# Kernel tuning notes

Measured on AMD Instinct MI355X. Metric: run time of the kernel, lower is better.

The kernel has to match this reference:

```python
import jax, jax.numpy as jnp
import numpy as np

N_TBINS = 1024
K = 8
B = 32768
IRF_SIGMA = 10.0
PEAK_FACTOR = 5.0
# IRF1DLayer: circular pad (pad_l=N//2, pad_r=N//2-1 for even N) then conv1d with
# flip(irf)  ==  circular convolution with irf followed by roll of -(N-1-N//2).
ROLL_C = N_TBINS - 1 - N_TBINS // 2  # 511


def _wrapped_gaussian(n, mu, sigma):
    # circ_shifted gaussian pulse: wrap tails around the domain, normalize to unit area
    t = np.arange(n, dtype=np.float64)
    g = np.zeros(n, dtype=np.float64)
    for s in (-n, 0, n):
        g += np.exp(-((t - mu + s) ** 2) / (2.0 * sigma ** 2))
    g /= g.sum()
    return jnp.asarray(g, dtype=jnp.float32)


def _circ_conv(x, irf):
    # faithful IRF1DLayer: circular convolution, recentered
    y = jnp.fft.irfft(jnp.fft.rfft(x, axis=-1) * jnp.fft.rfft(irf), n=N_TBINS, axis=-1)
    return jnp.roll(y, -ROLL_C, axis=-1)


def setup_inputs():
    key = jax.random.key(0)
    k1, k2, k3, k4 = jax.random.split(key, 4)
    illumination = _wrapped_gaussian(N_TBINS, N_TBINS // 2, 30.0)  # Gaussian1DLayer buffer
    irf = _wrapped_gaussian(N_TBINS, (N_TBINS - 1) // 2, IRF_SIGMA)
    photon_counts = jax.random.uniform(k1, (B,), jnp.float32, 10.0, 1000.0)
    sbrs = jax.random.uniform(k2, (B,), jnp.float32, 0.1, 1.0)
    bins = jax.random.randint(k3, (B,), 0, N_TBINS)
    cmat_weight = jax.random.normal(k4, (K, N_TBINS), jnp.float32) * 0.05  # Conv1d(k, n_tbins, 1) weight
    return {"illumination": illumination, "photon_counts": photon_counts,
            "sbrs": sbrs, "irf": irf, "cmat_weight": cmat_weight, "bins": bins}


def reference(illumination, photon_counts, sbrs, irf, cmat_weight, bins):
    n = N_TBINS
    inp = _circ_conv(jax.nn.relu(illumination), irf)          # [N] = irf(relu(illum))
    shifts = (bins % n).astype(jnp.int32)                     # [B]
    amb_per_bin = (photon_counts / sbrs) / n                  # [B]
    area = jnp.sum(inp)                                       # current_area
    scale = photon_counts / area                              # [B]
    scaled = inp[None, :] * scale[:, None]                    # [B, N]
    clamped = jnp.minimum(scaled, (PEAK_FACTOR * photon_counts)[:, None])
    offset = clamped + amb_per_bin[:, None]                   # [B, N]
    conv = _circ_conv(offset, irf)                            # [B, N] (batched FFT conv)
    # torch.roll(x, s): out[t] = x[(t - s) % N], vectorized over batch
    idx = (jnp.arange(n)[None, :] - shifts[:, None]) % n      # [B, N]
    shifted = jnp.take_along_axis(conv, idx, axis=1)          # [B, N]
    rate = jax.lax.stop_gradient(shifted)                     # torch.poisson detaches
    noisy = jax.random.poisson(jax.random.key(42), rate, shape=rate.shape).astype(jnp.float32)
    # cmat1D: Conv1d(in=n_tbins, out=k, kernel=1) on [B, N, 1] -> [B, K, 1]
    out = jnp.einsum('bn,kn->bk', noisy, cmat_weight)[..., None]
    return out
```

## Files before the change

### kernel.cpp

```cpp
#include <hip/hip_runtime.h>
#include <hip/hip_bf16.h>
#include <stdint.h>

#define N_T   1024
#define ROLLC 511
#define KCH   8
#define KN_LEV 48
#define RJ_LEV 24
#define CH_N  (2*KN_LEV + 4*RJ_LEV)

__device__ double   g_conv2[N_T];
__device__ double   g_area;
__device__ uint32_t g_chains[CH_N];
__device__ int      g_T;
__device__ float    g_ll5, g_aa5, g_bb5, g_inva5, g_vr5;

struct TF2 { uint32_t x, y; };

__device__ __forceinline__ TF2 tf2x32(uint32_t k0, uint32_t k1, uint32_t c0, uint32_t c1) {
  uint32_t ks2 = k0 ^ k1 ^ 0x1BD11BDAu;
  uint32_t x0 = c0 + k0, x1 = c1 + k1;
#define TFR(r) { x0 += x1; x1 = (x1 << (r)) | (x1 >> (32 - (r))); x1 ^= x0; }
  TFR(13) TFR(15) TFR(26) TFR(6)
  x0 += k1;  x1 += ks2 + 1u;
  TFR(17) TFR(29) TFR(16) TFR(24)
  x0 += ks2; x1 += k0 + 2u;
  TFR(13) TFR(15) TFR(26) TFR(6)
  x0 += k0;  x1 += k1 + 3u;
  TFR(17) TFR(29) TFR(16) TFR(24)
  x0 += k1;  x1 += ks2 + 4u;
  TFR(13) TFR(15) TFR(26) TFR(6)
  x0 += ks2; x1 += k0 + 5u;
#undef TFR
  return {x0, x1};
}

__device__ __forceinline__ float u01_from_key(uint32_t sk0, uint32_t sk1, uint32_t m) {
  TF2 r = tf2x32(sk0, sk1, 0u, m);
  uint32_t bits = r.x ^ r.y;
  return __uint_as_float((bits >> 9) | 0x3f800000u) - 1.0f;
}

__device__ __forceinline__ float lgamma_xla(float x) {
#pragma clang fp contract(off)
  float z = x - 1.0f;
  float sum = 1.0f;
  sum = sum + 676.5203681218851f     / (z + 1.0f);
  sum = sum + -1259.1392167224028f   / (z + 2.0f);
  sum = sum + 771.32342877765313f    / (z + 3.0f);
  sum = sum + -176.61502916214059f   / (z + 4.0f);
  sum = sum + 12.507343278686905f    / (z + 5.0f);
  sum = sum + -0.13857109526572012f  / (z + 6.0f);
  sum = sum + 9.9843695780195716e-6f / (z + 7.0f);
  sum = sum + 1.5056327351493116e-7f / (z + 8.0f);
  float t = 7.5f + z;
  float log_t = 2.0149030205422647f + log1pf(z / 7.5f);
  return 0.91893853320467274f + (z + 0.5f - t / log_t) * log_t + logf(sum);
}

__device__ __forceinline__ void rej_constants(float lam, float* ll, float* aa, float* bb,
                                              float* inva, float* vr) {
#pragma clang fp contract(off)
  *ll = logf(lam);
  float b = 0.931f + 2.53f * sqrtf(lam);
  float a = -0.059f + 0.02483f * b;
  *bb = b; *aa = a;
  *inva = 1.1239f + 1.1328f / (b - 3.4f);
  *vr = 0.9277f - 3.6224f / (b - 2.0f);
}

__device__ __forceinline__ bool rej_iter(float lam, float ll, float aa, float bb,
                                         float inva, float vr, float u, float v, float* kf) {
#pragma clang fp contract(off)
  float us = 0.5f - fabsf(u);
  float k = floorf((2.0f * aa / us + bb) * u + lam + 0.43f);
  *kf = k;
  if ((us >= 0.07f) && (v <= vr)) return true;
  if ((k < 0.0f) || ((us < 0.013f) && (v > us))) return false;
  float s = logf(v * inva / (aa / (us * us) + bb));
  float t = (-lam + k * ll) - lgamma_xla(k + 1.0f);
  return s <= t;
}

__device__ __forceinline__ float knuth_sample(float lam, uint32_t m, const uint32_t* __restrict__ ch) {
#pragma clang fp contract(off)
  const float neg = -lam;
  float lp = 0.0f;
  int k = 0;
#pragma unroll 1
  for (int j = 0; j < KN_LEV; ++j) {
    if (!(lp > neg)) break;
    ++k;
    float u = u01_from_key(ch[2*j], ch[2*j+1], m);
    lp = lp + logf(u);
  }
  return (float)(k - 1);
}

__global__ void __launch_bounds__(1024)
precompute_kernel(const float* __restrict__ illum, const float* __restrict__ irf,
                  uint32_t* __restrict__ wcount) {
  __shared__ double xs[N_T], irfs[N_T], inp[N_T];
  int t = threadIdx.x;
  xs[t]   = fmax((double)illum[t], 0.0);
  irfs[t] = (double)irf[t];
  __syncthreads();
  int tt = (t + ROLLC) & (N_T - 1);
  double acc = 0.0;
  for (int j = 0; j < N_T; ++j) acc += xs[j] * irfs[(tt - j) & (N_T - 1)];
  inp[t] = acc;
  __syncthreads();
  double acc2 = 0.0;
  for (int j = 0; j < N_T; ++j) acc2 += inp[j] * irfs[(tt - j) & (N_T - 1)];
  g_conv2[t] = acc2;
  if (t == 0) {
    g_T = 1;
    wcount[0] = 0u;
    double area = 0.0;
    for (int j = 0; j < N_T; ++j) area += inp[j];
    g_area = area;
    uint32_t r0 = 0u, r1 = 42u;
    for (int j = 0; j < KN_LEV; ++j) {
      TF2 sub = tf2x32(r0, r1, 0u, 1u);
      TF2 nxt = tf2x32(r0, r1, 0u, 0u);
      g_chains[2*j] = sub.x; g_chains[2*j+1] = sub.y;
      r0 = nxt.x; r1 = nxt.y;
    }
  } else if (t == 64) {
    uint32_t c0 = 0u, c1 = 42u;
    for (int j = 0; j < RJ_LEV; ++j) {
      TF2 nxt = tf2x32(c0, c1, 0u, 0u);
      TF2 s0  = tf2x32(c0, c1, 0u, 1u);
      TF2 s1  = tf2x32(c0, c1, 0u, 2u);
      int base = 2*KN_LEV + 4*j;
      g_chains[base]   = s0.x; g_chains[base+1] = s0.y;
      g_chains[base+2] = s1.x; g_chains[base+3] = s1.y;
      c0 = nxt.x; c1 = nxt.y;
    }
  } else if (t == 128) {
    float ll, aa, bb, inva, vr;
    rej_constants(1e5f, &ll, &aa, &bb, &inva, &vr);
    g_ll5 = ll; g_aa5 = aa; g_bb5 = bb; g_inva5 = inva; g_vr5 = vr;
  }
}

__global__ void __launch_bounds__(256)
t1_kernel(const float* __restrict__ photon, const float* __restrict__ sbr,
          const int* __restrict__ bins, uint32_t* __restrict__ wcount,
          uint2* __restrict__ recs, uint32_t cap) {
  __shared__ double conv2s[N_T];
  __shared__ uint2 lrec[N_T];
  __shared__ uint32_t lcount, gbase;
  const int b = blockIdx.x, tid = threadIdx.x;
  for (int i = tid; i < N_T; i += 256) conv2s[i] = g_conv2[i];
  if (tid == 0) lcount = 0u;
  __syncthreads();

  const float ph = photon[b], sb = sbr[b];
  const int   shift = bins[b] & (N_T - 1);
  const double scale = (double)ph / g_area;
  const float  r1f = ph / sb;
  const double amb = (double)r1f * (1.0 / 1024.0);
  const uint32_t sa0 = g_chains[2*KN_LEV+0], sa1 = g_chains[2*KN_LEV+1];
  const uint32_t sc0 = g_chains[2*KN_LEV+2], sc1 = g_chains[2*KN_LEV+3];
  const float ll5 = g_ll5, aa5 = g_aa5, bb5 = g_bb5, inva5 = g_inva5, vr5 = g_vr5;

  for (int i = 0; i < 4; ++i) {
    const int t   = tid + i * 256;
    const int src = (t - shift) & (N_T - 1);
    const float lam = (float)(scale * conv2s[src] + amb);
    float lamr, ll, aa, bbv, inva, vr;
    if (lam < 10.0f) { lamr = 1e5f; ll = ll5; aa = aa5; bbv = bb5; inva = inva5; vr = vr5; }
    else { lamr = lam; rej_constants(lam, &ll, &aa, &bbv, &inva, &vr); }
    const uint32_t m = (uint32_t)(b * N_T + t);
    float u = u01_from_key(sa0, sa1, m) - 0.5f;
    float v = u01_from_key(sc0, sc1, m);
    float kf;
    if (!rej_iter(lamr, ll, aa, bbv, inva, vr, u, v, &kf)) {
      uint32_t slot = atomicAdd(&lcount, 1u);
      lrec[slot] = make_uint2(m, __float_as_uint(lamr));
    }
  }
  __syncthreads();
  if (tid == 0) gbase = atomicAdd(wcount, lcount);
  __syncthreads();
  const uint32_t lc = lcount, base = gbase;
  for (uint32_t i = tid; i < lc; i += 256) {
    const uint32_t g = base + i;
    uint2 r = lrec[i];
    if (g < cap) {
      recs[g] = r;
    } else {
      const uint32_t m = r.x; const float lamr = __uint_as_float(r.y);
      float ll, aa, bbv, inva, vr;
      if (lamr == 1e5f) { ll = ll5; aa = aa5; bbv = bb5; inva = inva5; vr = vr5; }
      else rej_constants(lamr, &ll, &aa, &bbv, &inva, &vr);
      int jf = RJ_LEV;
#pragma unroll 1
      for (int j = 1; j < RJ_LEV; ++j) {
        const uint32_t* c = g_chains + 2*KN_LEV + 4*j;
        float uu = u01_from_key(c[0], c[1], m) - 0.5f;
        float vv = u01_from_key(c[2], c[3], m);
        float kk;
        if (rej_iter(lamr, ll, aa, bbv, inva, vr, uu, vv, &kk)) { jf = j + 1; break; }
      }
      atomicMax(&g_T, jf);
    }
  }
}

__global__ void __launch_bounds__(256)
t2_kernel(const uint32_t* __restrict__ wcount, const uint2* __restrict__ recs, uint32_t cap) {
  __shared__ uint32_t chs[4*RJ_LEV];
  __shared__ int bmax;
  const int tid = threadIdx.x;
  if (tid < 4*RJ_LEV) chs[tid] = g_chains[2*KN_LEV + tid];
  if (tid == 0) bmax = 1;
  __syncthreads();
  uint32_t n = *wcount; if (n > cap) n = cap;
  const float ll5 = g_ll5, aa5 = g_aa5, bb5 = g_bb5, inva5 = g_inva5, vr5 = g_vr5;
  int mymax = 1;
  for (uint32_t gi = blockIdx.x * 256u + tid; gi < n; gi += gridDim.x * 256u) {
    uint2 r = recs[gi];
    const uint32_t m = r.x; const float lamr = __uint_as_float(r.y);
    float ll, aa, bbv, inva, vr;
    if (lamr == 1e5f) { ll = ll5; aa = aa5; bbv = bb5; inva = inva5; vr = vr5; }
    else rej_constants(lamr, &ll, &aa, &bbv, &inva, &vr);
    int jf = RJ_LEV;
#pragma unroll 1
    for (int j = 1; j < RJ_LEV; ++j) {
      float uu = u01_from_key(chs[4*j], chs[4*j+1], m) - 0.5f;
      float vv = u01_from_key(chs[4*j+2], chs[4*j+3], m);
      float kk;
      if (rej_iter(lamr, ll, aa, bbv, inva, vr, uu, vv, &kk)) { jf = j + 1; break; }
    }
    mymax = max(mymax, jf);
  }
  for (int off = 32; off > 0; off >>= 1) mymax = max(mymax, __shfl_down(mymax, off, 64));
  if ((tid & 63) == 0) atomicMax(&bmax, mymax);
  __syncthreads();
  if (tid == 0) atomicMax(&g_T, bmax);
}

__global__ void __launch_bounds__(256)
sample_kernel(const float* __restrict__ photon, const float* __restrict__ sbr,
              const int* __restrict__ bins, const float* __restrict__ w,
              float* __restrict__ out) {
  __shared__ double conv2s[N_T];
  __shared__ uint32_t ch[CH_N];
  __shared__ float wred[4][KCH];
  const int b = blockIdx.x, tid = threadIdx.x;
  for (int i = tid; i < N_T; i += 256) conv2s[i] = g_conv2[i];
  if (tid < CH_N) ch[tid] = g_chains[tid];
  __syncthreads();

  const int   T  = g_T;
  const float ph = photon[b];
  const float sb = sbr[b];
  const int   shift = bins[b] & (N_T - 1);
  const double scale = (double)ph / g_area;
  const float  r1f = ph / sb;
  const double amb = (double)r1f * (1.0 / 1024.0);

  float acc[KCH];
#pragma unroll
  for (int k = 0; k < KCH; ++k) acc[k] = 0.0f;

  for (int i = 0; i < 4; ++i) {
    const int t   = tid + i * 256;
    const int src = (t - shift) & (N_T - 1);
    const float lam = (float)(scale * conv2s[src] + amb);
    const uint32_t m = (uint32_t)(b * N_T + t);
    float cnt;
    if (lam < 10.0f) {
      cnt = knuth_sample(lam, m, ch);
    } else {
      float ll, aa, bbv, inva, vr;
      rej_constants(lam, &ll, &aa, &bbv, &inva, &vr);
      float kout = -1.0f;
#pragma unroll 1
      for (int j = T - 1; j >= 0; --j) {
        const uint32_t* c = ch + 2*KN_LEV + 4*j;
        float u = u01_from_key(c[0], c[1], m) - 0.5f;
        float v = u01_from_key(c[2], c[3], m);
        float kf;
        if (rej_iter(lam, ll, aa, bbv, inva, vr, u, v, &kf)) { kout = kf; break; }
      }
      cnt = kout;
    }
#pragma unroll
    for (int k = 0; k < KCH; ++k) acc[k] += cnt * w[k * N_T + t];
  }

  const int lane = tid & 63, wv = tid >> 6;
#pragma unroll
  for (int k = 0; k < KCH; ++k) {
    float v = acc[k];
    for (int off = 32; off > 0; off >>= 1) v += __shfl_down(v, off, 64);
    if (lane == 0) wred[wv][k] = v;
  }
  __syncthreads();
  if (tid < KCH)
    out[b * KCH + tid] = wred[0][tid] + wred[1][tid] + wred[2][tid] + wred[3][tid];
}

extern "C" void kernel_launch(void* const* d_in, const int* in_sizes, int n_in,
                              void* d_out, int out_size, void* d_ws, size_t ws_size,
                              hipStream_t stream) {
  (void)n_in; (void)out_size;
  const float* illum  = (const float*)d_in[0];
  const float* photon = (const float*)d_in[1];
  const float* sbr    = (const float*)d_in[2];
  const float* irf    = (const float*)d_in[3];
  const float* w      = (const float*)d_in[4];
  const int*   bins   = (const int*)d_in[5];
  float* out = (float*)d_out;
  const int B = in_sizes[1];

  uint32_t* wcount = (uint32_t*)d_ws;
  uint2*    recs   = (uint2*)((char*)d_ws + 16);
  uint32_t  cap    = (ws_size > 16) ? (uint32_t)((ws_size - 16) / sizeof(uint2)) : 0u;

  precompute_kernel<<<1, 1024, 0, stream>>>(illum, irf, wcount);
  t1_kernel<<<B, 256, 0, stream>>>(photon, sbr, bins, wcount, recs, cap);
  t2_kernel<<<2048, 256, 0, stream>>>(wcount, recs, cap);
  sample_kernel<<<B, 256, 0, stream>>>(photon, sbr, bins, w, out);
}
```

Measured before the change: 1.179 ms.

## Compact divergent Poisson sampling work with wave-level appends and split precompute across blocks

Splits the single-block precompute into two multi-block kernels so the double-precision convolutions run on several CUs. The t1 pass now classifies rejection candidates with a cheap test and defers the expensive lgamma/log path to a compacted list. In the sampler, Knuth iterations run as compacted worklists in shared memory, and rejection-path elements are gathered separately, which reduces wave divergence. Wave-level ballot appends replace per-thread shared atomics. Fast __logf replaces logf in Knuth, which may change sampled counts at boundaries, and the extra block-wide syncs per Knuth level add overhead.

```diff
diff --git a/kernel.cpp b/kernel.cpp
--- a/kernel.cpp
+++ b/kernel.cpp
@@ -9,6 +9,7 @@
 #define RJ_LEV 24
 #define CH_N  (2*KN_LEV + 4*RJ_LEV)
 
+__device__ double   g_inp[N_T];
 __device__ double   g_conv2[N_T];
 __device__ double   g_area;
 __device__ uint32_t g_chains[CH_N];
@@ -69,6 +70,40 @@
   *vr = 0.9277f - 3.6224f / (b - 2.0f);
 }
 
+__device__ __forceinline__ void rej_quick_consts(float lam, float* aa, float* bb, float* vr) {
+#pragma clang fp contract(off)
+  float b = 0.931f + 2.53f * sqrtf(lam);
+  *bb = b;
+  *aa = -0.059f + 0.02483f * b;
+  *vr = 0.9277f - 3.6224f / (b - 2.0f);
+}
+
+__device__ __forceinline__ void rej_slow_consts(float lam, float bb, float* ll, float* inva) {
+#pragma clang fp contract(off)
+  *ll = logf(lam);
+  *inva = 1.1239f + 1.1328f / (bb - 3.4f);
+}
+
+__device__ __forceinline__ int ptrs_quick(float lamr, float aa, float bb, float vr,
+                                          float u, float v) {
+#pragma clang fp contract(off)
+  float us = 0.5f - fabsf(u);
+  float kf = floorf((2.0f * aa / us + bb) * u + lamr + 0.43f);
+  if ((us >= 0.07f) && (v <= vr)) return 1;
+  if ((kf < 0.0f) || ((us < 0.013f) && (v > us))) return -1;
+  return 0;
+}
+
+__device__ __forceinline__ bool ptrs_slow(float lamr, float ll, float aa, float bb,
+                                          float inva, float u, float v) {
+#pragma clang fp contract(off)
+  float us = 0.5f - fabsf(u);
+  float kf = floorf((2.0f * aa / us + bb) * u + lamr + 0.43f);
+  float s = logf(v * inva / (aa / (us * us) + bb));
+  float t = (-lamr + kf * ll) - lgamma_xla(kf + 1.0f);
+  return s <= t;
+}
+
 __device__ __forceinline__ bool rej_iter(float lam, float ll, float aa, float bb,
                                          float inva, float vr, float u, float v, float* kf) {
 #pragma clang fp contract(off)
@@ -82,65 +117,81 @@
   return s <= t;
 }
 
-__device__ __forceinline__ float knuth_sample(float lam, uint32_t m, const uint32_t* __restrict__ ch) {
-#pragma clang fp contract(off)
-  const float neg = -lam;
-  float lp = 0.0f;
-  int k = 0;
-#pragma unroll 1
-  for (int j = 0; j < KN_LEV; ++j) {
-    if (!(lp > neg)) break;
-    ++k;
-    float u = u01_from_key(ch[2*j], ch[2*j+1], m);
-    lp = lp + logf(u);
-  }
-  return (float)(k - 1);
-}
-
-__global__ void __launch_bounds__(1024)
-precompute_kernel(const float* __restrict__ illum, const float* __restrict__ irf,
-                  uint32_t* __restrict__ wcount) {
-  __shared__ double xs[N_T], irfs[N_T], inp[N_T];
-  int t = threadIdx.x;
-  xs[t]   = fmax((double)illum[t], 0.0);
-  irfs[t] = (double)irf[t];
-  __syncthreads();
-  int tt = (t + ROLLC) & (N_T - 1);
+__device__ __forceinline__ uint32_t wave_append(bool pred, uint32_t* counter) {
+  unsigned long long vote = __ballot(pred);
+  int lane = threadIdx.x & 63;
+  uint32_t base = 0;
+  int cnt = __popcll(vote);
+  if (cnt) {
+    int leader = __ffsll((unsigned long long)vote) - 1;
+    if (lane == leader) base = atomicAdd(counter, (uint32_t)cnt);
+    base = (uint32_t)__shfl((int)base, leader, 64);
+  }
+  return base + (uint32_t)__popcll(vote & ((1ull << lane) - 1ull));
+}
+
+__global__ void __launch_bounds__(128)
+pre1_kernel(const float* __restrict__ illum, const float* __restrict__ irf) {
+  __shared__ double xs[N_T], irfs[N_T];
+  const int tid = threadIdx.x;
+  for (int i = tid; i < N_T; i += 128) {
+    xs[i]   = fmax((double)illum[i], 0.0);
+    irfs[i] = (double)irf[i];
+  }
+  __syncthreads();
+  const int t  = blockIdx.x * 128 + tid;
+  const int tt = (t + ROLLC) & (N_T - 1);
   double acc = 0.0;
   for (int j = 0; j < N_T; ++j) acc += xs[j] * irfs[(tt - j) & (N_T - 1)];
-  inp[t] = acc;
-  __syncthreads();
-  double acc2 = 0.0;
-  for (int j = 0; j < N_T; ++j) acc2 += inp[j] * irfs[(tt - j) & (N_T - 1)];
-  g_conv2[t] = acc2;
-  if (t == 0) {
-    g_T = 1;
-    wcount[0] = 0u;
-    double area = 0.0;
-    for (int j = 0; j < N_T; ++j) area += inp[j];
-    g_area = area;
-    uint32_t r0 = 0u, r1 = 42u;
-    for (int j = 0; j < KN_LEV; ++j) {
-      TF2 sub = tf2x32(r0, r1, 0u, 1u);
-      TF2 nxt = tf2x32(r0, r1, 0u, 0u);
-      g_chains[2*j] = sub.x; g_chains[2*j+1] = sub.y;
-      r0 = nxt.x; r1 = nxt.y;
-    }
-  } else if (t == 64) {
-    uint32_t c0 = 0u, c1 = 42u;
-    for (int j = 0; j < RJ_LEV; ++j) {
-      TF2 nxt = tf2x32(c0, c1, 0u, 0u);
-      TF2 s0  = tf2x32(c0, c1, 0u, 1u);
-      TF2 s1  = tf2x32(c0, c1, 0u, 2u);
-      int base = 2*KN_LEV + 4*j;
-      g_chains[base]   = s0.x; g_chains[base+1] = s0.y;
-      g_chains[base+2] = s1.x; g_chains[base+3] = s1.y;
-      c0 = nxt.x; c1 = nxt.y;
-    }
-  } else if (t == 128) {
-    float ll, aa, bb, inva, vr;
-    rej_constants(1e5f, &ll, &aa, &bb, &inva, &vr);
-    g_ll5 = ll; g_aa5 = aa; g_bb5 = bb; g_inva5 = inva; g_vr5 = vr;
+  g_inp[t] = acc;
+}
+
+__global__ void __launch_bounds__(128)
+pre2_kernel(const float* __restrict__ irf, uint32_t* __restrict__ wcount) {
+  __shared__ double inps[N_T], irfs[N_T];
+  const int tid = threadIdx.x;
+  if (blockIdx.x < 8) {
+    for (int i = tid; i < N_T; i += 128) {
+      inps[i] = g_inp[i];
+      irfs[i] = (double)irf[i];
+    }
+    __syncthreads();
+    const int t  = blockIdx.x * 128 + tid;
+    const int tt = (t + ROLLC) & (N_T - 1);
+    double acc = 0.0;
+    for (int j = 0; j < N_T; ++j) acc += inps[j] * irfs[(tt - j) & (N_T - 1)];
+    g_conv2[t] = acc;
+  } else {
+    if (tid == 0) {
+      g_T = 1;
+      wcount[0] = 0u;
+      double area = 0.0;
+      for (int j = 0; j < N_T; ++j) area += g_inp[j];
+      g_area = area;
+    } else if (tid == 1) {
+      uint32_t r0 = 0u, r1 = 42u;
+      for (int j = 0; j < KN_LEV; ++j) {
+        TF2 sub = tf2x32(r0, r1, 0u, 1u);
+        TF2 nxt = tf2x32(r0, r1, 0u, 0u);
+        g_chains[2*j] = sub.x; g_chains[2*j+1] = sub.y;
+        r0 = nxt.x; r1 = nxt.y;
+      }
+    } else if (tid == 2) {
+      uint32_t c0 = 0u, c1 = 42u;
+      for (int j = 0; j < RJ_LEV; ++j) {
+        TF2 nxt = tf2x32(c0, c1, 0u, 0u);
+        TF2 s0  = tf2x32(c0, c1, 0u, 1u);
+        TF2 s1  = tf2x32(c0, c1, 0u, 2u);
+        int base = 2*KN_LEV + 4*j;
+        g_chains[base]   = s0.x; g_chains[base+1] = s0.y;
+        g_chains[base+2] = s1.x; g_chains[base+3] = s1.y;
+        c0 = nxt.x; c1 = nxt.y;
+      }
+    } else if (tid == 3) {
+      float ll, aa, bb, inva, vr;
+      rej_constants(1e5f, &ll, &aa, &bb, &inva, &vr);
+      g_ll5 = ll; g_aa5 = aa; g_bb5 = bb; g_inva5 = inva; g_vr5 = vr;
+    }
   }
 }
 
@@ -148,12 +199,12 @@
 t1_kernel(const float* __restrict__ photon, const float* __restrict__ sbr,
           const int* __restrict__ bins, uint32_t* __restrict__ wcount,
           uint2* __restrict__ recs, uint32_t cap) {
-  __shared__ double conv2s[N_T];
-  __shared__ uint2 lrec[N_T];
-  __shared__ uint32_t lcount, gbase;
+  __shared__ uint2    lrec[N_T];
+  __shared__ uint32_t amb_m[N_T];
+  __shared__ float    amb_u[N_T], amb_v[N_T], amb_lam[N_T];
+  __shared__ uint32_t lcount, acount, gbase;
   const int b = blockIdx.x, tid = threadIdx.x;
-  for (int i = tid; i < N_T; i += 256) conv2s[i] = g_conv2[i];
-  if (tid == 0) lcount = 0u;
+  if (tid == 0) { lcount = 0u; acount = 0u; }
   __syncthreads();
 
   const float ph = photon[b], sb = sbr[b];
@@ -164,24 +215,50 @@
   const uint32_t sa0 = g_chains[2*KN_LEV+0], sa1 = g_chains[2*KN_LEV+1];
   const uint32_t sc0 = g_chains[2*KN_LEV+2], sc1 = g_chains[2*KN_LEV+3];
   const float ll5 = g_ll5, aa5 = g_aa5, bb5 = g_bb5, inva5 = g_inva5, vr5 = g_vr5;
-
-  for (int i = 0; i < 4; ++i) {
-    const int t   = tid + i * 256;
+  const uint32_t mbase = (uint32_t)b << 10;
+
+  for (int i2 = 0; i2 < 4; ++i2) {
+    const int t   = tid + (i2 << 8);
     const int src = (t - shift) & (N_T - 1);
-    const float lam = (float)(scale * conv2s[src] + amb);
-    float lamr, ll, aa, bbv, inva, vr;
-    if (lam < 10.0f) { lamr = 1e5f; ll = ll5; aa = aa5; bbv = bb5; inva = inva5; vr = vr5; }
-    else { lamr = lam; rej_constants(lam, &ll, &aa, &bbv, &inva, &vr); }
-    const uint32_t m = (uint32_t)(b * N_T + t);
+    const float lam = (float)(scale * g_conv2[src] + amb);
+    float lamr, aa, bbv, vr;
+    if (lam < 10.0f) { lamr = 1e5f; aa = aa5; bbv = bb5; vr = vr5; }
+    else { lamr = lam; rej_quick_consts(lam, &aa, &bbv, &vr); }
+    const uint32_t m = mbase + (uint32_t)t;
     float u = u01_from_key(sa0, sa1, m) - 0.5f;
     float v = u01_from_key(sc0, sc1, m);
-    float kf;
-    if (!rej_iter(lamr, ll, aa, bbv, inva, vr, u, v, &kf)) {
-      uint32_t slot = atomicAdd(&lcount, 1u);
-      lrec[slot] = make_uint2(m, __float_as_uint(lamr));
-    }
-  }
-  __syncthreads();
+    int cls = ptrs_quick(lamr, aa, bbv, vr, u, v);
+    bool surv = (cls < 0);
+    bool ambg = (cls == 0);
+    uint32_t sS = wave_append(surv, &lcount);
+    if (surv) lrec[sS] = make_uint2(m, __float_as_uint(lamr));
+    uint32_t sA = wave_append(ambg, &acount);
+    if (ambg) { amb_m[sA] = m; amb_u[sA] = u; amb_v[sA] = v; amb_lam[sA] = lamr; }
+  }
+  __syncthreads();
+
+  const uint32_t na = acount;
+  const uint32_t naPad = (na + 255u) & ~255u;
+  for (uint32_t i = tid; i < naPad; i += 256) {
+    bool active = (i < na);
+    bool surv = false;
+    uint32_t m = 0; float lamr = 0.f;
+    if (active) {
+      m = amb_m[i]; lamr = amb_lam[i];
+      float u = amb_u[i], v = amb_v[i];
+      float ll, aa, bbv, inva;
+      if (lamr == 1e5f) { ll = ll5; aa = aa5; bbv = bb5; inva = inva5; }
+      else { rej_quick_consts(lamr, &aa, &bbv, &inva ); float vv;
+             float b2 = 0.931f + 2.53f * sqrtf(lamr);
+             bbv = b2; aa = -0.059f + 0.02483f * b2;
+             rej_slow_consts(lamr, bbv, &ll, &inva); (void)vv; }
+      surv = !ptrs_slow(lamr, ll, aa, bbv, inva, u, v);
+    }
+    uint32_t sS = wave_append(surv, &lcount);
+    if (surv) lrec[sS] = make_uint2(m, __float_as_uint(lamr));
+  }
+  __syncthreads();
+
   if (tid == 0) gbase = atomicAdd(wcount, lcount);
   __syncthreads();
   const uint32_t lc = lcount, base = gbase;
@@ -246,35 +323,91 @@
 sample_kernel(const float* __restrict__ photon, const float* __restrict__ sbr,
               const int* __restrict__ bins, const float* __restrict__ w,
               float* __restrict__ out) {
-  __shared__ double conv2s[N_T];
   __shared__ uint32_t ch[CH_N];
+  __shared__ float lamS[N_T];
+  __shared__ float lpS[N_T];
+  __shared__ float cntS[N_T];
+  __shared__ uint16_t listA[N_T], listB[N_T], rejL[N_T];
+  __shared__ uint32_t nA, nB, nRej;
   __shared__ float wred[4][KCH];
   const int b = blockIdx.x, tid = threadIdx.x;
-  for (int i = tid; i < N_T; i += 256) conv2s[i] = g_conv2[i];
   if (tid < CH_N) ch[tid] = g_chains[tid];
-  __syncthreads();
-
-  const int   T  = g_T;
-  const float ph = photon[b];
-  const float sb = sbr[b];
+  if (tid == 0) { nA = 0u; nB = 0u; nRej = 0u; }
+  __syncthreads();
+
+  const float ph = photon[b], sb = sbr[b];
   const int   shift = bins[b] & (N_T - 1);
   const double scale = (double)ph / g_area;
   const float  r1f = ph / sb;
   const double amb = (double)r1f * (1.0 / 1024.0);
-
-  float acc[KCH];
-#pragma unroll
-  for (int k = 0; k < KCH; ++k) acc[k] = 0.0f;
-
-  for (int i = 0; i < 4; ++i) {
-    const int t   = tid + i * 256;
+  const uint32_t mbase = (uint32_t)b << 10;
+
+  for (int i2 = 0; i2 < 4; ++i2) {
+    const int t   = tid + (i2 << 8);
     const int src = (t - shift) & (N_T - 1);
-    const float lam = (float)(scale * conv2s[src] + amb);
-    const uint32_t m = (uint32_t)(b * N_T + t);
-    float cnt;
-    if (lam < 10.0f) {
-      cnt = knuth_sample(lam, m, ch);
-    } else {
+    const float lam = (float)(scale * g_conv2[src] + amb);
+    lamS[t] = lam;
+    const bool kn = (lam < 10.0f);
+    float lp0 = 0.0f;
+    if (kn) {
+      float u = u01_from_key(ch[0], ch[1], mbase + (uint32_t)t);
+      lp0 = __logf(u);
+    }
+    lpS[t] = lp0;
+    uint32_t sA = wave_append(kn, &nA);
+    if (kn) listA[sA] = (uint16_t)t;
+    uint32_t sR = wave_append(!kn, &nRej);
+    if (!kn) rejL[sR] = (uint16_t)t;
+  }
+
+  {
+    uint16_t* cur = listA; uint32_t* curn = &nA;
+    uint16_t* nxt = listB; uint32_t* nxtn = &nB;
+    int j = 1;
+    while (true) {
+      __syncthreads();
+      const uint32_t n = *curn;
+      if (n == 0u) break;
+      if (j >= KN_LEV) {
+        for (uint32_t i = tid; i < n; i += 256) cntS[cur[i]] = (float)(KN_LEV - 1);
+        break;
+      }
+      if (tid == 0) *nxtn = 0u;
+      __syncthreads();
+      const uint32_t k0 = ch[2*j], k1 = ch[2*j+1];
+      const uint32_t nPad = (n + 255u) & ~255u;
+      for (uint32_t i = tid; i < nPad; i += 256) {
+        bool alive = false;
+        uint16_t t16 = 0; float lpn = 0.0f;
+        if (i < n) {
+          t16 = cur[i];
+          const float neg = -lamS[t16];
+          const float lp = lpS[t16];
+          if (lp > neg) {
+            float u = u01_from_key(k0, k1, mbase + (uint32_t)t16);
+            lpn = lp + __logf(u);
+            alive = true;
+          } else {
+            cntS[t16] = (float)(j - 1);
+          }
+        }
+        uint32_t slot = wave_append(alive, nxtn);
+        if (alive) { nxt[slot] = t16; lpS[t16] = lpn; }
+      }
+      { uint16_t* tp = cur; cur = nxt; nxt = tp; }
+      { uint32_t* tp = curn; curn = nxtn; nxtn = tp; }
+      ++j;
+    }
+  }
+  __syncthreads();
+
+  {
+    const int T = g_T;
+    const uint32_t nr = nRej;
+    for (uint32_t i = tid; i < nr; i += 256) {
+      const uint16_t t16 = rejL[i];
+      const float lam = lamS[t16];
+      const uint32_t m = mbase + (uint32_t)t16;
       float ll, aa, bbv, inva, vr;
       rej_constants(lam, &ll, &aa, &bbv, &inva, &vr);
       float kout = -1.0f;
@@ -286,12 +419,20 @@
         float kf;
         if (rej_iter(lam, ll, aa, bbv, inva, vr, u, v, &kf)) { kout = kf; break; }
       }
-      cnt = kout;
-    }
+      cntS[t16] = kout;
+    }
+  }
+  __syncthreads();
+
+  float acc[KCH];
 #pragma unroll
-    for (int k = 0; k < KCH; ++k) acc[k] += cnt * w[k * N_T + t];
-  }
-
+  for (int k = 0; k < KCH; ++k) acc[k] = 0.0f;
+  for (int i2 = 0; i2 < 4; ++i2) {
+    const int t = tid + (i2 << 8);
+    const float c = cntS[t];
+#pragma unroll
+    for (int k = 0; k < KCH; ++k) acc[k] += c * w[k * N_T + t];
+  }
   const int lane = tid & 63, wv = tid >> 6;
 #pragma unroll
   for (int k = 0; k < KCH; ++k) {
@@ -321,7 +462,8 @@
   uint2*    recs   = (uint2*)((char*)d_ws + 16);
   uint32_t  cap    = (ws_size > 16) ? (uint32_t)((ws_size - 16) / sizeof(uint2)) : 0u;
 
-  precompute_kernel<<<1, 1024, 0, stream>>>(illum, irf, wcount);
+  pre1_kernel<<<8, 128, 0, stream>>>(illum, irf);
+  pre2_kernel<<<9, 128, 0, stream>>>(irf, wcount);
   t1_kernel<<<B, 256, 0, stream>>>(photon, sbr, bins, wcount, recs, cap);
   t2_kernel<<<2048, 256, 0, stream>>>(wcount, recs, cap);
   sample_kernel<<<B, 256, 0, stream>>>(photon, sbr, bins, w, out);
```

Measured after the change: 1.151 ms. -2.3%, faster.
